# Kernel optimization log

Measured on AMD Instinct MI355X. Metric: run time of the kernel, lower is better.

The kernel has to match this reference:

```python
import jax, jax.numpy as jnp
import numpy as np

N = 50000
E = 1600000
IN_DIM = 128
H = 8
D = 16  # out_dim per head


def setup_inputs() -> dict:
    key = jax.random.key(0)
    ks = jax.random.split(key, 9)
    h = jax.random.normal(ks[0], (N, IN_DIM), dtype=jnp.float32)
    src = jax.random.randint(ks[1], (E,), 0, N, dtype=jnp.int32)
    dst = jax.random.randint(ks[2], (E,), 0, N, dtype=jnp.int32)
    s = 1.0 / np.sqrt(IN_DIM)
    WQ = jax.random.uniform(ks[3], (IN_DIM, H * D), jnp.float32, -s, s)
    WK = jax.random.uniform(ks[4], (IN_DIM, H * D), jnp.float32, -s, s)
    WV = jax.random.uniform(ks[5], (IN_DIM, H * D), jnp.float32, -s, s)
    bQ = jax.random.uniform(ks[6], (H * D,), jnp.float32, -s, s)
    bK = jax.random.uniform(ks[7], (H * D,), jnp.float32, -s, s)
    bV = jax.random.uniform(ks[8], (H * D,), jnp.float32, -s, s)
    return {"h": h, "src": src, "dst": dst, "WQ": WQ, "WK": WK, "WV": WV,
            "bQ": bQ, "bK": bK, "bV": bV}


def reference(h, src, dst, WQ, WK, WV, bQ, bK, bV):
    # Node projections -> [N, H, D]
    Q = (h @ WQ + bQ).reshape(-1, H, D)
    K = (h @ WK + bK).reshape(-1, H, D)
    V = (h @ WV + bV).reshape(-1, H, D)
    # Edge scores: dot(K[src], Q[dst]) per head, scaled+clamped exp -> [E, H]
    scale = jnp.float32(np.sqrt(D))
    score = jnp.exp(jnp.clip(jnp.sum(K[src] * Q[dst], axis=-1) / scale, -5.0, 5.0))
    # Scatter-sum to destination nodes
    wV = jax.ops.segment_sum(score[:, :, None] * V[src], dst, num_segments=N)  # [N, H, D]
    z = jax.ops.segment_sum(score, dst, num_segments=N)  # [N, H]
    return wV / z[:, :, None]
```

## Files before the change

kernel.cpp:

```cpp
#include <hip/hip_runtime.h>

#define N_NODES 50000
#define N_PAD   50048
#define N_EDGES 1600000
#define HD 128
#define CHUNK 4096
#define NCHUNK ((N_EDGES + CHUNK - 1) / CHUNK)
#define NBUCKET ((N_NODES + 127) / 128)

typedef __attribute__((ext_vector_type(8))) short short8;
typedef __attribute__((ext_vector_type(4))) float floatx4;

union U4S8 { uint4 u; short8 s; };

__device__ __forceinline__ unsigned short f2bf(float f) {
    unsigned u = __float_as_uint(f);
    unsigned r = (u + 0x7fffu + ((u >> 16) & 1u)) >> 16;
    return (unsigned short)r;
}

__global__ __launch_bounds__(256) void k_chunkhist(
    const int* __restrict__ dst, int* __restrict__ chunkhist, int* __restrict__ btot,
    const float* __restrict__ WQ, const float* __restrict__ WK, const float* __restrict__ WV,
    unsigned short* __restrict__ Wf) {
    int t = threadIdx.x, c = blockIdx.x;
    if (c >= NCHUNK) {
        int tid = (c - NCHUNK) * 256 + t;
        int lane = tid & 63;
        int kstep = (tid >> 6) & 3;
        int ntile = tid >> 8;
        int g = ntile >> 3;
        int col = (ntile & 7) * 16 + (lane & 15);
        int k0 = kstep * 32 + (lane >> 4) * 8;
        const float* W = (g == 0) ? WQ : (g == 1) ? WK : WV;
        unsigned short r[8];
#pragma unroll
        for (int j = 0; j < 8; ++j)
            r[j] = f2bf(W[(size_t)(k0 + j) * HD + col]);
        *(uint4*)(Wf + (size_t)tid * 8) = *(uint4*)r;
        return;
    }
    __shared__ int hist[NBUCKET];
    for (int i = t; i < NBUCKET; i += 256) hist[i] = 0;
    __syncthreads();
    int e0 = c * CHUNK;
    int cnt = min(CHUNK, N_EDGES - e0);
    const uint4* d4 = (const uint4*)(dst + e0);
    int cnt4 = cnt >> 2;
    for (int i = t; i < cnt4; i += 256) {
        uint4 v = d4[i];
        atomicAdd(&hist[v.x >> 7], 1);
        atomicAdd(&hist[v.y >> 7], 1);
        atomicAdd(&hist[v.z >> 7], 1);
        atomicAdd(&hist[v.w >> 7], 1);
    }
    __syncthreads();
    for (int i = t; i < NBUCKET; i += 256) {
        int v = hist[i];
        chunkhist[c * NBUCKET + i] = v;
        if (v) atomicAdd(&btot[i], v);
    }
}

__global__ __launch_bounds__(256) void k_choff(const int* __restrict__ chunkhist,
                                               const int* __restrict__ btot,
                                               int* __restrict__ bucket_ptr,
                                               int* __restrict__ chunkoff) {
    int b = blockIdx.x, t = threadIdx.x;
    int x = 0;
    for (int i = t; i < NBUCKET; i += 256)
        if (i < b) x += btot[i];
    __shared__ int red[256];
    red[t] = x;
    __syncthreads();
    for (int off = 128; off > 0; off >>= 1) {
        if (t < off) red[t] += red[t + off];
        __syncthreads();
    }
    int base = red[0];
    if (t == 0) {
        bucket_ptr[b] = base;
        if (b == NBUCKET - 1) bucket_ptr[NBUCKET] = base + btot[b];
    }
    const int PER = (NCHUNK + 255) / 256;
    int c0 = t * PER;
    int v[PER];
    int s = 0;
#pragma unroll
    for (int i = 0; i < PER; ++i) {
        int c = c0 + i;
        v[i] = (c < NCHUNK) ? chunkhist[c * NBUCKET + b] : 0;
        s += v[i];
    }
    __shared__ int part[256];
    part[t] = s;
    __syncthreads();
    for (int off = 1; off < 256; off <<= 1) {
        int y = (t >= off) ? part[t - off] : 0;
        __syncthreads();
        part[t] += y;
        __syncthreads();
    }
    int run = base + part[t] - s;
#pragma unroll
    for (int i = 0; i < PER; ++i) {
        int c = c0 + i;
        if (c < NCHUNK) { chunkoff[c * NBUCKET + b] = run; run += v[i]; }
    }
}

__global__ __launch_bounds__(256) void k_scatter(const int* __restrict__ src,
                                                 const int* __restrict__ dst,
                                                 const int* __restrict__ chunkoff,
                                                 int* __restrict__ packed) {
    __shared__ int cur[NBUCKET];
    int t = threadIdx.x, c = blockIdx.x;
    for (int i = t; i < NBUCKET; i += 256) cur[i] = chunkoff[c * NBUCKET + i];
    __syncthreads();
    int e0 = c * CHUNK;
    int cnt = min(CHUNK, N_EDGES - e0);
    const uint4* d4 = (const uint4*)(dst + e0);
    const uint4* s4 = (const uint4*)(src + e0);
    int cnt4 = cnt >> 2;
    for (int i = t; i < cnt4; i += 256) {
        uint4 d = d4[i];
        uint4 s = s4[i];
        int pos;
        pos = atomicAdd(&cur[d.x >> 7], 1); packed[pos] = (s.x << 7) | (d.x & 127);
        pos = atomicAdd(&cur[d.y >> 7], 1); packed[pos] = (s.y << 7) | (d.y & 127);
        pos = atomicAdd(&cur[d.z >> 7], 1); packed[pos] = (s.z << 7) | (d.z & 127);
        pos = atomicAdd(&cur[d.w >> 7], 1); packed[pos] = (s.w << 7) | (d.w & 127);
    }
}

__global__ __launch_bounds__(256) void k_finalize(const int* __restrict__ bucket_ptr,
                                                  const int* __restrict__ packed,
                                                  int* __restrict__ row_ptr,
                                                  int* __restrict__ col_src) {
    __shared__ int hist[128], part[128], cur[128];
    int b = blockIdx.x, t = threadIdx.x;
    if (t < 128) hist[t] = 0;
    __syncthreads();
    int ebeg = bucket_ptr[b], eend = bucket_ptr[b + 1];
    int m = eend - ebeg;
    for (int i = t; i < m; i += 256)
        atomicAdd(&hist[packed[ebeg + i] & 127], 1);
    __syncthreads();
    int v = 0;
    if (t < 128) { v = hist[t]; part[t] = v; }
    __syncthreads();
    for (int off = 1; off < 128; off <<= 1) {
        int x = 0;
        if (t < 128 && t >= off) x = part[t - off];
        __syncthreads();
        if (t < 128) part[t] += x;
        __syncthreads();
    }
    if (t < 128) {
        int excl = part[t] - v;
        int node = b * 128 + t;
        if (node < N_NODES) row_ptr[node] = ebeg + excl;
        if (node == N_NODES - 1) row_ptr[N_NODES] = eend;
        cur[t] = ebeg + excl;
    }
    __syncthreads();
    for (int i = t; i < m; i += 256) {
        int p = packed[ebeg + i];
        int pos = atomicAdd(&cur[p & 127], 1);
        col_src[pos] = p >> 7;
    }
}


__global__ __launch_bounds__(256) void proj_mfma(
    const float* __restrict__ h, const unsigned short* __restrict__ Wf,
    const float* __restrict__ bQ, const float* __restrict__ bK, const float* __restrict__ bV,
    float* __restrict__ Qo, unsigned short* __restrict__ Kb, unsigned short* __restrict__ Vb) {
    int t = threadIdx.x;
    int w = t >> 6;
    int l = t & 63;
    int row0 = blockIdx.x * 64 + w * 16;
    int arow = row0 + (l & 15);
    int akoff = (l >> 4) * 8;
    bool rowok = arow < N_NODES;

    short8 a[4];
#pragma unroll
    for (int ks = 0; ks < 4; ++ks) {
        unsigned short r[8];
        if (rowok) {
            const float4* ap = (const float4*)(h + (size_t)arow * HD + ks * 32 + akoff);
            float4 f0 = ap[0], f1 = ap[1];
            r[0] = f2bf(f0.x); r[1] = f2bf(f0.y); r[2] = f2bf(f0.z); r[3] = f2bf(f0.w);
            r[4] = f2bf(f1.x); r[5] = f2bf(f1.y); r[6] = f2bf(f1.z); r[7] = f2bf(f1.w);
        } else {
#pragma unroll
            for (int j = 0; j < 8; ++j) r[j] = 0;
        }
        a[ks] = *(short8*)r;
    }

    int orow0 = row0 + (l >> 4) * 4;
#pragma unroll
    for (int nt = 0; nt < 24; ++nt) {
        floatx4 acc = (floatx4){0.f, 0.f, 0.f, 0.f};
#pragma unroll
        for (int ks = 0; ks < 4; ++ks) {
            U4S8 u;
            u.u = *(const uint4*)(Wf + ((size_t)(nt * 4 + ks) * 64 + l) * 8);
            acc = __builtin_amdgcn_mfma_f32_16x16x32_bf16(a[ks], u.s, acc, 0, 0, 0);
        }
        int g = nt >> 3;
        int cc = (nt & 7) * 16 + (l & 15);
        float bias = (g == 0) ? bQ[cc] : (g == 1) ? bK[cc] : bV[cc];
#pragma unroll
        for (int r = 0; r < 4; ++r) {
            int grow = orow0 + r;
            if (grow < N_NODES) {
                float val = acc[r] + bias;
                if (g == 0)      Qo[(size_t)grow * HD + cc] = val;
                else if (g == 1) Kb[(size_t)grow * HD + cc] = f2bf(val);
                else             Vb[(size_t)grow * HD + cc] = f2bf(val);
            }
        }
    }
}


__device__ __forceinline__ float blo(unsigned u) { return __uint_as_float(u << 16); }
__device__ __forceinline__ float bhi(unsigned u) { return __uint_as_float(u & 0xffff0000u); }

__global__ __launch_bounds__(256) void attn_kernel(
    const float* __restrict__ Q,
    const unsigned short* __restrict__ Kb, const unsigned short* __restrict__ Vb,
    const int* __restrict__ row_ptr, const int* __restrict__ col_src,
    float* __restrict__ out, int nbase, int nend) {
    int n = nbase + blockIdx.x * 4 + (threadIdx.x >> 6);
    if (n >= nend) return;
    int l = threadIdx.x & 63;
    int o = l >> 3;
    int p = l & 7;

    const float4* Qv = (const float4*)(Q + (size_t)n * HD + p * 16);
    float4 q0 = Qv[0], q1 = Qv[1], q2 = Qv[2], q3 = Qv[3];

    float acc[16];
#pragma unroll
    for (int j = 0; j < 16; ++j) acc[j] = 0.f;
    float z = 0.f;

    int beg = row_ptr[n], end = row_ptr[n + 1];

    for (int base = beg; base < end; base += 64) {
        int mm = min(64, end - base);
        int e_l = col_src[(base + l < end) ? (base + l) : beg];
        int steps = (mm + 7) >> 3;

        int s0 = __shfl(e_l, o);
        const uint4* Kp = (const uint4*)(Kb + (size_t)s0 * HD + p * 16);
        const uint4* Vp = (const uint4*)(Vb + (size_t)s0 * HD + p * 16);
        uint4 ka = Kp[0], kb = Kp[1], va = Vp[0], vb = Vp[1];

        for (int i = 0; i < steps; ++i) {
            uint4 nka = ka, nkb = kb, nva = va, nvb = vb;
            if (i + 1 < steps) {
                int s1 = __shfl(e_l, 8 * (i + 1) + o);
                const uint4* Kn = (const uint4*)(Kb + (size_t)s1 * HD + p * 16);
                const uint4* Vn = (const uint4*)(Vb + (size_t)s1 * HD + p * 16);
                nka = Kn[0]; nkb = Kn[1]; nva = Vn[0]; nvb = Vn[1];
            }
            float dot = blo(ka.x) * q0.x + bhi(ka.x) * q0.y
                      + blo(ka.y) * q0.z + bhi(ka.y) * q0.w
                      + blo(ka.z) * q1.x + bhi(ka.z) * q1.y
                      + blo(ka.w) * q1.z + bhi(ka.w) * q1.w
                      + blo(kb.x) * q2.x + bhi(kb.x) * q2.y
                      + blo(kb.y) * q2.z + bhi(kb.y) * q2.w
                      + blo(kb.z) * q3.x + bhi(kb.z) * q3.y
                      + blo(kb.w) * q3.z + bhi(kb.w) * q3.w;
            float sc = __expf(fminf(fmaxf(dot * 0.25f, -5.f), 5.f));
            if (8 * i + o >= mm) sc = 0.f;
            acc[0]  = fmaf(sc, blo(va.x), acc[0]);
            acc[1]  = fmaf(sc, bhi(va.x), acc[1]);
            acc[2]  = fmaf(sc, blo(va.y), acc[2]);
            acc[3]  = fmaf(sc, bhi(va.y), acc[3]);
            acc[4]  = fmaf(sc, blo(va.z), acc[4]);
            acc[5]  = fmaf(sc, bhi(va.z), acc[5]);
            acc[6]  = fmaf(sc, blo(va.w), acc[6]);
            acc[7]  = fmaf(sc, bhi(va.w), acc[7]);
            acc[8]  = fmaf(sc, blo(vb.x), acc[8]);
            acc[9]  = fmaf(sc, bhi(vb.x), acc[9]);
            acc[10] = fmaf(sc, blo(vb.y), acc[10]);
            acc[11] = fmaf(sc, bhi(vb.y), acc[11]);
            acc[12] = fmaf(sc, blo(vb.z), acc[12]);
            acc[13] = fmaf(sc, bhi(vb.z), acc[13]);
            acc[14] = fmaf(sc, blo(vb.w), acc[14]);
            acc[15] = fmaf(sc, bhi(vb.w), acc[15]);
            z += sc;
            ka = nka; kb = nkb; va = nva; vb = nvb;
        }
    }

#pragma unroll
    for (int j = 0; j < 16; ++j) {
        acc[j] += __shfl_xor(acc[j], 8);
        acc[j] += __shfl_xor(acc[j], 16);
        acc[j] += __shfl_xor(acc[j], 32);
    }
    z += __shfl_xor(z, 8);
    z += __shfl_xor(z, 16);
    z += __shfl_xor(z, 32);

    if (o == 0) {
        float inv = 1.f / z;
        float4* O = (float4*)(out + (size_t)n * HD + p * 16);
        O[0] = (float4){acc[0] * inv,  acc[1] * inv,  acc[2] * inv,  acc[3] * inv};
        O[1] = (float4){acc[4] * inv,  acc[5] * inv,  acc[6] * inv,  acc[7] * inv};
        O[2] = (float4){acc[8] * inv,  acc[9] * inv,  acc[10] * inv, acc[11] * inv};
        O[3] = (float4){acc[12] * inv, acc[13] * inv, acc[14] * inv, acc[15] * inv};
    }
}


static inline char* align256(char* p) {
    return (char*)(((uintptr_t)p + 255) & ~(uintptr_t)255);
}

extern "C" void kernel_launch(void* const* d_in, const int* in_sizes, int n_in,
                              void* d_out, int out_size, void* d_ws, size_t ws_size,
                              hipStream_t stream) {
    const float* h  = (const float*)d_in[0];
    const int*   src = (const int*)d_in[1];
    const int*   dst = (const int*)d_in[2];
    const float* WQ = (const float*)d_in[3];
    const float* WK = (const float*)d_in[4];
    const float* WV = (const float*)d_in[5];
    const float* bQ = (const float*)d_in[6];
    const float* bK = (const float*)d_in[7];
    const float* bV = (const float*)d_in[8];
    float* out = (float*)d_out;

    char* p = (char*)d_ws;
    float* Q = (float*)p;                    p += (size_t)N_PAD * HD * 4;
    unsigned short* Kb = (unsigned short*)p; p += (size_t)N_PAD * HD * 2;
    unsigned short* Vb = (unsigned short*)p; p += (size_t)N_PAD * HD * 2;
    unsigned short* Wf = (unsigned short*)p; p += (size_t)24 * 4 * 64 * 8 * 2;
    p = align256(p);
    int* row_ptr    = (int*)p;               p += (N_NODES + 2) * 4;
    p = align256(p);
    int* bucket_ptr = (int*)p;               p += (NBUCKET + 1) * 4;
    p = align256(p);
    int* btot       = (int*)p;               p += NBUCKET * 4;
    p = align256(p);
    int* chunkhist  = (int*)p;               p += (size_t)NCHUNK * NBUCKET * 4;
    p = align256(p);
    int* chunkoff   = (int*)p;               p += (size_t)NCHUNK * NBUCKET * 4;
    p = align256(p);
    int* packed     = (int*)p;               p += (size_t)N_EDGES * 4;
    p = align256(p);
    int* col_src    = (int*)p;               p += (size_t)N_EDGES * 4;

    (void)hipMemsetAsync(btot, 0, NBUCKET * sizeof(int), stream);
    k_chunkhist<<<NCHUNK + 24, 256, 0, stream>>>(dst, chunkhist, btot, WQ, WK, WV, Wf);
    k_choff<<<NBUCKET, 256, 0, stream>>>(chunkhist, btot, bucket_ptr, chunkoff);
    k_scatter<<<NCHUNK, 256, 0, stream>>>(src, dst, chunkoff, packed);
    k_finalize<<<NBUCKET, 256, 0, stream>>>(bucket_ptr, packed, row_ptr, col_src);
    proj_mfma<<<N_PAD / 64, 256, 0, stream>>>(h, Wf, bQ, bK, bV, Q, Kb, Vb);
    const int T1 = 16668, T2 = 33336;
    attn_kernel<<<(T1 + 3) / 4, 256, 0, stream>>>(Q, Kb, Vb, row_ptr, col_src, out, 0, T1);
    attn_kernel<<<(T2 - T1 + 3) / 4, 256, 0, stream>>>(Q, Kb, Vb, row_ptr, col_src, out, T1, T2);
    attn_kernel<<<(N_NODES - T2 + 3) / 4, 256, 0, stream>>>(Q, Kb, Vb, row_ptr, col_src, out, T2, N_NODES);
}
```

Measured before the change: 269.5 us.

## Use head-major interleaved K/V layout and one block per head in attention

```diff
diff --git a/kernel.cpp b/kernel.cpp
--- a/kernel.cpp
+++ b/kernel.cpp
@@ -175,7 +175,7 @@
 __global__ __launch_bounds__(256) void proj_mfma(
     const float* __restrict__ h, const unsigned short* __restrict__ Wf,
     const float* __restrict__ bQ, const float* __restrict__ bK, const float* __restrict__ bV,
-    float* __restrict__ Qo, unsigned short* __restrict__ Kb, unsigned short* __restrict__ Vb) {
+    float* __restrict__ Qh, unsigned short* __restrict__ KV) {
     int t = threadIdx.x;
     int w = t >> 6;
     int l = t & 63;
@@ -211,16 +211,18 @@
             acc = __builtin_amdgcn_mfma_f32_16x16x32_bf16(a[ks], u.s, acc, 0, 0, 0);
         }
         int g = nt >> 3;
-        int cc = (nt & 7) * 16 + (l & 15);
-        float bias = (g == 0) ? bQ[cc] : (g == 1) ? bK[cc] : bV[cc];
+        int head = nt & 7;
+        int ci = l & 15;
+        float bias = (g == 0) ? bQ[head * 16 + ci] : (g == 1) ? bK[head * 16 + ci] : bV[head * 16 + ci];
 #pragma unroll
         for (int r = 0; r < 4; ++r) {
             int grow = orow0 + r;
             if (grow < N_NODES) {
                 float val = acc[r] + bias;
-                if (g == 0)      Qo[(size_t)grow * HD + cc] = val;
-                else if (g == 1) Kb[(size_t)grow * HD + cc] = f2bf(val);
-                else             Vb[(size_t)grow * HD + cc] = f2bf(val);
+                size_t node_off = (size_t)head * N_PAD + grow;
+                if (g == 0)      Qh[node_off * 16 + ci] = val;
+                else if (g == 1) KV[node_off * 32 + ci] = f2bf(val);
+                else             KV[node_off * 32 + 16 + ci] = f2bf(val);
             }
         }
     }
@@ -231,92 +233,81 @@
 __device__ __forceinline__ float bhi(unsigned u) { return __uint_as_float(u & 0xffff0000u); }
 
 __global__ __launch_bounds__(256) void attn_kernel(
-    const float* __restrict__ Q,
-    const unsigned short* __restrict__ Kb, const unsigned short* __restrict__ Vb,
+    const float* __restrict__ Qh, const unsigned short* __restrict__ KV,
     const int* __restrict__ row_ptr, const int* __restrict__ col_src,
-    float* __restrict__ out, int nbase, int nend) {
-    int n = nbase + blockIdx.x * 4 + (threadIdx.x >> 6);
-    if (n >= nend) return;
+    float* __restrict__ out) {
+    int head = blockIdx.x & 7;
+    int grp  = blockIdx.x >> 3;
+    int w = threadIdx.x >> 6;
+    int n = grp * 4 + w;
     int l = threadIdx.x & 63;
-    int o = l >> 3;
-    int p = l & 7;
-
-    const float4* Qv = (const float4*)(Q + (size_t)n * HD + p * 16);
-    float4 q0 = Qv[0], q1 = Qv[1], q2 = Qv[2], q3 = Qv[3];
-
-    float acc[16];
-#pragma unroll
-    for (int j = 0; j < 16; ++j) acc[j] = 0.f;
+    int s = l >> 2;
+    int j = l & 3;
+
+    const float4* qp = (const float4*)(Qh + ((size_t)head * N_PAD + n) * 16 + (j & 1) * 8);
+    float4 qa = qp[0], qb = qp[1];
+
+    float acc[8];
+#pragma unroll
+    for (int k = 0; k < 8; ++k) acc[k] = 0.f;
     float z = 0.f;
 
     int beg = row_ptr[n], end = row_ptr[n + 1];
+    const unsigned short* KVh = KV + (size_t)head * N_PAD * 32;
 
     for (int base = beg; base < end; base += 64) {
         int mm = min(64, end - base);
         int e_l = col_src[(base + l < end) ? (base + l) : beg];
-        int steps = (mm + 7) >> 3;
-
-        int s0 = __shfl(e_l, o);
-        const uint4* Kp = (const uint4*)(Kb + (size_t)s0 * HD + p * 16);
-        const uint4* Vp = (const uint4*)(Vb + (size_t)s0 * HD + p * 16);
-        uint4 ka = Kp[0], kb = Kp[1], va = Vp[0], vb = Vp[1];
+        int steps = (mm + 15) >> 4;
+
+        int s0 = __shfl(e_l, s);
+        uint4 kv = *(const uint4*)(KVh + (size_t)s0 * 32 + j * 8);
 
         for (int i = 0; i < steps; ++i) {
-            uint4 nka = ka, nkb = kb, nva = va, nvb = vb;
+            uint4 nkv = kv;
             if (i + 1 < steps) {
-                int s1 = __shfl(e_l, 8 * (i + 1) + o);
-                const uint4* Kn = (const uint4*)(Kb + (size_t)s1 * HD + p * 16);
-                const uint4* Vn = (const uint4*)(Vb + (size_t)s1 * HD + p * 16);
-                nka = Kn[0]; nkb = Kn[1]; nva = Vn[0]; nvb = Vn[1];
+                int s1 = __shfl(e_l, 16 * (i + 1) + s);
+                nkv = *(const uint4*)(KVh + (size_t)s1 * 32 + j * 8);
             }
-            float dot = blo(ka.x) * q0.x + bhi(ka.x) * q0.y
-                      + blo(ka.y) * q0.z + bhi(ka.y) * q0.w
-                      + blo(ka.z) * q1.x + bhi(ka.z) * q1.y
-                      + blo(ka.w) * q1.z + bhi(ka.w) * q1.w
-                      + blo(kb.x) * q2.x + bhi(kb.x) * q2.y
-                      + blo(kb.y) * q2.z + bhi(kb.y) * q2.w
-                      + blo(kb.z) * q3.x + bhi(kb.z) * q3.y
-                      + blo(kb.w) * q3.z + bhi(kb.w) * q3.w;
-            float sc = __expf(fminf(fmaxf(dot * 0.25f, -5.f), 5.f));
-            if (8 * i + o >= mm) sc = 0.f;
-            acc[0]  = fmaf(sc, blo(va.x), acc[0]);
-            acc[1]  = fmaf(sc, bhi(va.x), acc[1]);
-            acc[2]  = fmaf(sc, blo(va.y), acc[2]);
-            acc[3]  = fmaf(sc, bhi(va.y), acc[3]);
-            acc[4]  = fmaf(sc, blo(va.z), acc[4]);
-            acc[5]  = fmaf(sc, bhi(va.z), acc[5]);
-            acc[6]  = fmaf(sc, blo(va.w), acc[6]);
-            acc[7]  = fmaf(sc, bhi(va.w), acc[7]);
-            acc[8]  = fmaf(sc, blo(vb.x), acc[8]);
-            acc[9]  = fmaf(sc, bhi(vb.x), acc[9]);
-            acc[10] = fmaf(sc, blo(vb.y), acc[10]);
-            acc[11] = fmaf(sc, bhi(vb.y), acc[11]);
-            acc[12] = fmaf(sc, blo(vb.z), acc[12]);
-            acc[13] = fmaf(sc, bhi(vb.z), acc[13]);
-            acc[14] = fmaf(sc, blo(vb.w), acc[14]);
-            acc[15] = fmaf(sc, bhi(vb.w), acc[15]);
+            float v0 = blo(kv.x), v1 = bhi(kv.x), v2 = blo(kv.y), v3 = bhi(kv.y);
+            float v4 = blo(kv.z), v5 = bhi(kv.z), v6 = blo(kv.w), v7 = bhi(kv.w);
+            float d = v0 * qa.x + v1 * qa.y + v2 * qa.z + v3 * qa.w
+                    + v4 * qb.x + v5 * qb.y + v6 * qb.z + v7 * qb.w;
+            d += __shfl_xor(d, 1);
+            float dd = __shfl_xor(d, 2);
+            float kd = (l & 2) ? dd : d;
+            float sc = __expf(fminf(fmaxf(kd * 0.25f, -5.f), 5.f));
+            if (16 * i + s >= mm) sc = 0.f;
+            acc[0] = fmaf(sc, v0, acc[0]);
+            acc[1] = fmaf(sc, v1, acc[1]);
+            acc[2] = fmaf(sc, v2, acc[2]);
+            acc[3] = fmaf(sc, v3, acc[3]);
+            acc[4] = fmaf(sc, v4, acc[4]);
+            acc[5] = fmaf(sc, v5, acc[5]);
+            acc[6] = fmaf(sc, v6, acc[6]);
+            acc[7] = fmaf(sc, v7, acc[7]);
             z += sc;
-            ka = nka; kb = nkb; va = nva; vb = nvb;
+            kv = nkv;
         }
     }
 
 #pragma unroll
-    for (int j = 0; j < 16; ++j) {
-        acc[j] += __shfl_xor(acc[j], 8);
-        acc[j] += __shfl_xor(acc[j], 16);
-        acc[j] += __shfl_xor(acc[j], 32);
-    }
+    for (int k = 0; k < 8; ++k) {
+        acc[k] += __shfl_xor(acc[k], 4);
+        acc[k] += __shfl_xor(acc[k], 8);
+        acc[k] += __shfl_xor(acc[k], 16);
+        acc[k] += __shfl_xor(acc[k], 32);
+    }
+    z += __shfl_xor(z, 4);
     z += __shfl_xor(z, 8);
     z += __shfl_xor(z, 16);
     z += __shfl_xor(z, 32);
 
-    if (o == 0) {
+    if (s == 0 && (l & 2)) {
         float inv = 1.f / z;
-        float4* O = (float4*)(out + (size_t)n * HD + p * 16);
-        O[0] = (float4){acc[0] * inv,  acc[1] * inv,  acc[2] * inv,  acc[3] * inv};
-        O[1] = (float4){acc[4] * inv,  acc[5] * inv,  acc[6] * inv,  acc[7] * inv};
-        O[2] = (float4){acc[8] * inv,  acc[9] * inv,  acc[10] * inv, acc[11] * inv};
-        O[3] = (float4){acc[12] * inv, acc[13] * inv, acc[14] * inv, acc[15] * inv};
+        float* O = out + (size_t)n * HD + head * 16 + (j & 1) * 8;
+        ((float4*)O)[0] = (float4){acc[0] * inv, acc[1] * inv, acc[2] * inv, acc[3] * inv};
+        ((float4*)O)[1] = (float4){acc[4] * inv, acc[5] * inv, acc[6] * inv, acc[7] * inv};
     }
 }
 
@@ -340,9 +331,8 @@
     float* out = (float*)d_out;
 
     char* p = (char*)d_ws;
-    float* Q = (float*)p;                    p += (size_t)N_PAD * HD * 4;
-    unsigned short* Kb = (unsigned short*)p; p += (size_t)N_PAD * HD * 2;
-    unsigned short* Vb = (unsigned short*)p; p += (size_t)N_PAD * HD * 2;
+    float* Qh = (float*)p;                   p += (size_t)8 * N_PAD * 16 * 4;
+    unsigned short* KV = (unsigned short*)p; p += (size_t)8 * N_PAD * 32 * 2;
     unsigned short* Wf = (unsigned short*)p; p += (size_t)24 * 4 * 64 * 8 * 2;
     p = align256(p);
     int* row_ptr    = (int*)p;               p += (N_NODES + 2) * 4;
@@ -364,9 +354,6 @@
     k_choff<<<NBUCKET, 256, 0, stream>>>(chunkhist, btot, bucket_ptr, chunkoff);
     k_scatter<<<NCHUNK, 256, 0, stream>>>(src, dst, chunkoff, packed);
     k_finalize<<<NBUCKET, 256, 0, stream>>>(bucket_ptr, packed, row_ptr, col_src);
-    proj_mfma<<<N_PAD / 64, 256, 0, stream>>>(h, Wf, bQ, bK, bV, Q, Kb, Vb);
-    const int T1 = 16668, T2 = 33336;
-    attn_kernel<<<(T1 + 3) / 4, 256, 0, stream>>>(Q, Kb, Vb, row_ptr, col_src, out, 0, T1);
-    attn_kernel<<<(T2 - T1 + 3) / 4, 256, 0, stream>>>(Q, Kb, Vb, row_ptr, col_src, out, T1, T2);
-    attn_kernel<<<(N_NODES - T2 + 3) / 4, 256, 0, stream>>>(Q, Kb, Vb, row_ptr, col_src, out, T2, N_NODES);
-}
+    proj_mfma<<<N_PAD / 64, 256, 0, stream>>>(h, Wf, bQ, bK, bV, Qh, KV);
+    attn_kernel<<<(N_NODES / 4) * 8, 256, 0, stream>>>(Qh, KV, row_ptr, col_src, out);
+}
```

Result: slower. 339.4 us (+25.9%).
